# Kernel tuning notes

Hardware: AMD Instinct MI355X
Metric: run time of the kernel (lower is better)

The kernel has to match this reference:

```python
import jax, jax.numpy as jnp
import numpy as np

D_MODEL = 1024
NUM_HEADS = 16


def setup_inputs() -> dict:
    key = jax.random.key(0)
    ks = jax.random.split(key, 9)
    B, S, D = 4, 1024, D_MODEL
    scale = 1.0 / np.sqrt(D)
    inp = {
        "query": jax.random.normal(ks[0], (B, S, D), dtype=jnp.float32),
        "key": jax.random.normal(ks[1], (B, S, D), dtype=jnp.float32),
        "value": jax.random.normal(ks[2], (B, S, D), dtype=jnp.float32),
        # causal mask: 1 = attend, 0 = blocked (masked_fill where mask==0)
        "mask": jnp.tril(jnp.ones((S, S), dtype=jnp.int32))[None, None, :, :],
        "Wq": jax.random.normal(ks[3], (D, D), dtype=jnp.float32) * scale,
        "Wk": jax.random.normal(ks[4], (D, D), dtype=jnp.float32) * scale,
        "Wv": jax.random.normal(ks[5], (D, D), dtype=jnp.float32) * scale,
        "Wo": jax.random.normal(ks[6], (D, D), dtype=jnp.float32) * scale,
        "bo": jnp.zeros((D,), dtype=jnp.float32),
    }
    return inp


def reference(query, key, value, mask, Wq, Wk, Wv, Wo, bo):
    B, S, D = query.shape
    H = NUM_HEADS
    dk = D // H
    # torch Linear: y = x @ W.T  (bias=False for q/k/v)
    def proj(x, W):
        return (x @ W.T).reshape(B, S, H, dk).transpose(0, 2, 1, 3)  # [B,H,S,dk]

    Q = proj(query, Wq)
    K = proj(key, Wk)
    V = proj(value, Wv)

    scores = jnp.einsum("bhqd,bhkd->bhqk", Q, K) / jnp.sqrt(
        jnp.asarray(dk, dtype=jnp.float32)
    )
    scores = jnp.where(mask == 0, jnp.asarray(-1e9, scores.dtype), scores)
    attn = jax.nn.softmax(scores, axis=-1)
    out = jnp.einsum("bhqk,bhkd->bhqd", attn, V)  # [B,H,S,dk]
    out = out.transpose(0, 2, 1, 3).reshape(B, S, D)
    return out @ Wo.T + bo
```

## Files before the change

### kernel.cpp

```cpp
#include <hip/hip_runtime.h>

typedef __bf16 bf16x8 __attribute__((ext_vector_type(8)));
typedef short  s16x8  __attribute__((ext_vector_type(8)));
typedef float  f32x4  __attribute__((ext_vector_type(4)));
typedef float  f32x16 __attribute__((ext_vector_type(16)));
typedef unsigned int   u32x4 __attribute__((ext_vector_type(4)));
typedef unsigned short u16x4 __attribute__((ext_vector_type(4)));

#define NH   16
#define HD   64
#define SEQ  1024
#define DM   1024
#define NB   4
#define MTOT 4096

#define SCALE_L2E 0.1803368801111204f

__device__ __forceinline__ unsigned short f2bf(float f) {
    unsigned u = __builtin_bit_cast(unsigned, f);
    u += 0x7FFFu + ((u >> 16) & 1u);
    return (unsigned short)(u >> 16);
}

__device__ __forceinline__ s16x8 cvt8(f32x4 a, f32x4 b) {
    s16x8 r;
    r[0] = (short)f2bf(a[0]); r[1] = (short)f2bf(a[1]);
    r[2] = (short)f2bf(a[2]); r[3] = (short)f2bf(a[3]);
    r[4] = (short)f2bf(b[0]); r[5] = (short)f2bf(b[1]);
    r[6] = (short)f2bf(b[2]); r[7] = (short)f2bf(b[3]);
    return r;
}

__device__ __forceinline__ unsigned short bfbits(float x) {
    __bf16 h = (__bf16)x;
    return __builtin_bit_cast(unsigned short, h);
}
__device__ __forceinline__ float bf2f(unsigned short b) {
    unsigned u = (unsigned)b << 16;
    return __builtin_bit_cast(float, u);
}
__device__ __forceinline__ unsigned pk2(float a, float b) {
    return (unsigned)bfbits(a) | ((unsigned)bfbits(b) << 16);
}

__device__ __forceinline__ void gl16(const void* g, void* l) {
    __builtin_amdgcn_global_load_lds(
        (const __attribute__((address_space(1))) unsigned int*)g,
        (__attribute__((address_space(3))) unsigned int*)l, 16, 0, 0);
}

__device__ __forceinline__ bf16x8 ldfrag(const char* base, int row, int cb) {
    return __builtin_bit_cast(bf16x8,
        *(const s16x8*)(base + row * 128 + (cb ^ ((row & 7) << 4))));
}

__global__ __launch_bounds__(256)
void cvt_kernel(const float* __restrict__ q, const float* __restrict__ k,
                const float* __restrict__ v, const float* __restrict__ wq,
                const float* __restrict__ wk, const float* __restrict__ wv,
                unsigned short* __restrict__ dq, unsigned short* __restrict__ dk,
                unsigned short* __restrict__ dv, unsigned short* __restrict__ dwq,
                unsigned short* __restrict__ dwk, unsigned short* __restrict__ dwv)
{
    const int id = blockIdx.x;
    const float* s; unsigned short* d; int off; float scl = 1.0f;
    if (id < 6144) {
        const int t = id >> 11; off = id & 2047;
        s = (t == 0) ? q : (t == 1) ? k : v;
        d = (t == 0) ? dq : (t == 1) ? dk : dv;
    } else {
        const int w = (id - 6144) >> 9; off = (id - 6144) & 511;
        s = (w == 0) ? wq : (w == 1) ? wk : wv;
        d = (w == 0) ? dwq : (w == 1) ? dwk : dwv;
        if (w == 0) scl = SCALE_L2E;
    }
    const int idx = off * 2048 + threadIdx.x * 8;
    const f32x4* sp = (const f32x4*)(s + idx);
    *(s16x8*)(d + idx) = cvt8(sp[0] * scl, sp[1] * scl);
}

__device__ __forceinline__ void stage_half(const unsigned short* __restrict__ src,
                                           int grow0, int k0, char* ldsdst, int tid)
{
    const int wv  = tid >> 6;
    const int row = tid >> 3;
    const int scx = ((tid & 7) * 16) ^ ((row & 7) << 4);
    gl16((const char*)(src + (size_t)(grow0 + row) * DM + k0) + scx,
         ldsdst + wv * 1024);
    gl16((const char*)(src + (size_t)(grow0 + 64 + row) * DM + k0) + scx,
         ldsdst + 8192 + wv * 1024);
}

__device__ __forceinline__ void stage128x64(const unsigned short* __restrict__ src,
                                            int row0, int k0, char* lds, int tid)
{
    const int wv  = tid >> 6;
    const int row = tid >> 3;
    const int scx = ((tid & 7) * 16) ^ ((row & 7) << 4);
    #pragma unroll
    for (int i = 0; i < 4; ++i) {
        const char* g = (const char*)(src + (size_t)(row0 + i * 32 + row) * DM + k0) + scx;
        gl16(g, lds + i * 4096 + wv * 1024);
    }
}

__device__ __forceinline__ void loadB256(const float* __restrict__ src, int row0,
                                         int k0, int tid, f32x4 v[8])
{
    const int ce = (tid & 7) * 8;
    #pragma unroll
    for (int i = 0; i < 4; ++i) {
        const int row = (tid >> 3) + i * 32;
        const f32x4* p = (const f32x4*)(src + (size_t)(row0 + row) * DM + k0 + ce);
        v[2 * i] = p[0]; v[2 * i + 1] = p[1];
    }
}
__device__ __forceinline__ void writeB256(char* dst, int tid, const f32x4 v[8])
{
    const int cB = (tid & 7) * 16;
    #pragma unroll
    for (int i = 0; i < 4; ++i) {
        const int row = (tid >> 3) + i * 32;
        *(s16x8*)(dst + row * 128 + (cB ^ ((row & 7) << 4))) = cvt8(v[2 * i], v[2 * i + 1]);
    }
}

__global__ __launch_bounds__(512, 2)
void proj_kernel(const unsigned short* __restrict__ Xq,
                 const unsigned short* __restrict__ Xk,
                 const unsigned short* __restrict__ Xv,
                 const unsigned short* __restrict__ Wq,
                 const unsigned short* __restrict__ Wk,
                 const unsigned short* __restrict__ Wv,
                 unsigned short* __restrict__ Qo, unsigned short* __restrict__ Ko,
                 unsigned short* __restrict__ VTo)
{
    __shared__ char smem[147456];

    const int bid = blockIdx.x;
    const int swz = (bid & 7) * 24 + (bid >> 3);
    const int which = swz >> 6;
    const int rem   = swz & 63;
    const int m0 = (rem >> 2) * 256, n0 = (rem & 3) * 256;

    const unsigned short* X = (which == 0) ? Xq : (which == 1) ? Xk : Xv;
    const unsigned short* W = (which == 0) ? Wq : (which == 1) ? Wk : Wv;

    const int tid = threadIdx.x, lane = tid & 63, wv = tid >> 6;
    const int wrB = (wv >> 2) * 128;
    const int wcB = (wv & 3) * 64;
    const int fr = lane & 15, hi = lane >> 4, r4 = hi * 4;

    f32x4 acc[8][4];
    #pragma unroll
    for (int i = 0; i < 8; ++i)
        #pragma unroll
        for (int j = 0; j < 4; ++j) acc[i][j] = (f32x4){0.f, 0.f, 0.f, 0.f};

    stage_half(X, m0,       0, smem +     0, tid);
    stage_half(X, m0 + 128, 0, smem + 16384, tid);
    stage_half(W, n0,       0, smem + 32768, tid);
    stage_half(W, n0 + 128, 0, smem + 49152, tid);

    for (int t = 0; t < 16; ++t) {
        const char* Abuf = smem + (t & 1) * 65536;
        const char* Bbuf = Abuf + 32768;
        char* nb = smem + ((t & 1) ^ 1) * 65536;
        const int kn = (t + 1) * 64;

        bf16x8 af[2][4], bf01[2][2], bf23[2][2];

        if (t < 15) {
            stage_half(X, m0, kn, nb, tid);
            asm volatile("s_waitcnt vmcnt(2)" ::: "memory");
        } else {
            asm volatile("s_waitcnt vmcnt(0)" ::: "memory");
        }
        __builtin_amdgcn_s_barrier();
        __builtin_amdgcn_sched_barrier(0);
        #pragma unroll
        for (int ks = 0; ks < 2; ++ks) {
            const int cb = ks * 64 + hi * 16;
            #pragma unroll
            for (int mt = 0; mt < 4; ++mt) af[ks][mt] = ldfrag(Abuf, wrB + mt * 16 + fr, cb);
            #pragma unroll
            for (int nt = 0; nt < 2; ++nt) bf01[ks][nt] = ldfrag(Bbuf, wcB + nt * 16 + fr, cb);
        }
        __builtin_amdgcn_s_setprio(1);
        #pragma unroll
        for (int ks = 0; ks < 2; ++ks)
            #pragma unroll
            for (int mt = 0; mt < 4; ++mt)
                #pragma unroll
                for (int nt = 0; nt < 2; ++nt)
                    acc[mt][nt] = __builtin_amdgcn_mfma_f32_16x16x32_bf16(
                        af[ks][mt], bf01[ks][nt], acc[mt][nt], 0, 0, 0);
        __builtin_amdgcn_s_setprio(0);

        __builtin_amdgcn_s_barrier();
        __builtin_amdgcn_sched_barrier(0);
        #pragma unroll
        for (int ks = 0; ks < 2; ++ks) {
            const int cb = ks * 64 + hi * 16;
            #pragma unroll
            for (int nt = 0; nt < 2; ++nt) bf23[ks][nt] = ldfrag(Bbuf, wcB + 32 + nt * 16 + fr, cb);
        }
        if (t < 15) stage_half(X, m0 + 128, kn, nb + 16384, tid);
        __builtin_amdgcn_s_setprio(1);
        #pragma unroll
        for (int ks = 0; ks < 2; ++ks)
            #pragma unroll
            for (int mt = 0; mt < 4; ++mt)
                #pragma unroll
                for (int nt = 0; nt < 2; ++nt)
                    acc[mt][nt + 2] = __builtin_amdgcn_mfma_f32_16x16x32_bf16(
                        af[ks][mt], bf23[ks][nt], acc[mt][nt + 2], 0, 0, 0);
        __builtin_amdgcn_s_setprio(0);

        __builtin_amdgcn_s_barrier();
        __builtin_amdgcn_sched_barrier(0);
        #pragma unroll
        for (int ks = 0; ks < 2; ++ks) {
            const int cb = ks * 64 + hi * 16;
            #pragma unroll
            for (int mt = 0; mt < 4; ++mt) af[ks][mt] = ldfrag(Abuf, wrB + 64 + mt * 16 + fr, cb);
        }
        if (t < 15) stage_half(W, n0, kn, nb + 32768, tid);
        __builtin_amdgcn_s_setprio(1);
        #pragma unroll
        for (int ks = 0; ks < 2; ++ks)
            #pragma unroll
            for (int mt = 0; mt < 4; ++mt)
                #pragma unroll
                for (int nt = 0; nt < 2; ++nt)
                    acc[mt + 4][nt] = __builtin_amdgcn_mfma_f32_16x16x32_bf16(
                        af[ks][mt], bf01[ks][nt], acc[mt + 4][nt], 0, 0, 0);
        __builtin_amdgcn_s_setprio(0);

        __builtin_amdgcn_s_barrier();
        __builtin_amdgcn_sched_barrier(0);
        if (t < 15) stage_half(W, n0 + 128, kn, nb + 49152, tid);
        __builtin_amdgcn_s_setprio(1);
        #pragma unroll
        for (int ks = 0; ks < 2; ++ks)
            #pragma unroll
            for (int mt = 0; mt < 4; ++mt)
                #pragma unroll
                for (int nt = 0; nt < 2; ++nt)
                    acc[mt + 4][nt + 2] = __builtin_amdgcn_mfma_f32_16x16x32_bf16(
                        af[ks][mt], bf23[ks][nt], acc[mt + 4][nt + 2], 0, 0, 0);
        __builtin_amdgcn_s_setprio(0);
    }

    __syncthreads();

    unsigned short* sE = (unsigned short*)(smem + wv * 18432);
    #pragma unroll
    for (int mt = 0; mt < 8; ++mt)
        #pragma unroll
        for (int nt = 0; nt < 4; ++nt)
            #pragma unroll
            for (int r = 0; r < 4; ++r) {
                const int row = mt * 16 + r4 + r;
                const int col = nt * 16 + fr;
                sE[row * 72 + (col ^ (((row >> 3) & 7) << 3))] = f2bf(acc[mt][nt][r]);
            }
    asm volatile("s_waitcnt lgkmcnt(0)" ::: "memory");

    const int hB    = (n0 + wcB) >> 6;
    const int sbase = m0 + wrB;
    const int bb    = sbase >> 10;
    const int srow0 = sbase & 1023;

    if (which < 2) {
        unsigned short* QK = ((which == 0) ? Qo : Ko)
            + (((size_t)(bb * NH + hB)) * SEQ + srow0) * HD;
        #pragma unroll
        for (int it = 0; it < 16; ++it) {
            const int idx = it * 64 + lane;
            const int row = idx >> 3, c = idx & 7;
            s16x8 v = *(const s16x8*)&sE[row * 72 + ((c ^ ((row >> 3) & 7)) * 8)];
            *(s16x8*)(QK + (size_t)row * HD + c * 8) = v;
        }
    } else {
        const int t0 = srow0 >> 6;
        unsigned short* VD = VTo + (size_t)(bb * NH + hB) * (SEQ * HD)
                                 + (size_t)t0 * 4096;
        #pragma unroll
        for (int it = 0; it < 16; ++it) {
            const int tt = it >> 3, r = it & 7;
            const int sb = tt * 64 + (r >> 1) * 16 + (lane >> 5) * 8;
            const int d  = (lane & 31) + (r & 1) * 32;
            s16x8 v;
            #pragma unroll
            for (int j = 0; j < 8; ++j) {
                const int row = sb + j;
                v[j] = (short)sE[row * 72 + (d ^ (((row >> 3) & 7) << 3))];
            }
            *(s16x8*)(VD + (size_t)(tt * 8 + r) * 512 + lane * 8) = v;
        }
    }
}

__global__ __launch_bounds__(256)
void outproj_kernel(const unsigned short* __restrict__ A,
                    const float* __restrict__ Wo,
                    const float* __restrict__ bo,
                    float* __restrict__ Cout)
{
    const int bid = blockIdx.x;
    const int swz = (bid & 7) * 32 + (bid >> 3);
    const int m0 = (swz >> 3) * 128, n0 = (swz & 7) * 128;

    __shared__ char sA[2][16384];
    __shared__ char sB[2][16384];

    const int tid = threadIdx.x, lane = tid & 63, wv = tid >> 6;
    const int wr = (wv >> 1) * 64, wc = (wv & 1) * 64;
    const int fr = lane & 15, hi = lane >> 4, r4 = hi * 4;

    f32x4 acc[4][4];
    #pragma unroll
    for (int i = 0; i < 4; ++i)
        #pragma unroll
        for (int j = 0; j < 4; ++j) acc[i][j] = (f32x4){0.f, 0.f, 0.f, 0.f};

    f32x4 bv[8];
    loadB256(Wo, n0, 0, tid, bv);
    stage128x64(A, m0, 0, sA[0], tid);
    writeB256(sB[0], tid, bv);
    __syncthreads();

    for (int kt = 0; kt < 16; ++kt) {
        const int cur = kt & 1;
        if (kt < 15) {
            loadB256(Wo, n0, (kt + 1) * 64, tid, bv);
            stage128x64(A, m0, (kt + 1) * 64, sA[cur ^ 1], tid);
            asm volatile("s_waitcnt vmcnt(12)" ::: "memory");
        } else {
            asm volatile("s_waitcnt vmcnt(0)" ::: "memory");
        }
        __builtin_amdgcn_s_barrier();
        __builtin_amdgcn_sched_barrier(0);
        #pragma unroll
        for (int ks = 0; ks < 2; ++ks) {
            const int cb = ks * 64 + hi * 16;
            bf16x8 af[4], bfm[4];
            #pragma unroll
            for (int mt = 0; mt < 4; ++mt)
                af[mt] = ldfrag(sA[cur], wr + mt * 16 + fr, cb);
            #pragma unroll
            for (int nt = 0; nt < 4; ++nt)
                bfm[nt] = ldfrag(sB[cur], wc + nt * 16 + fr, cb);
            #pragma unroll
            for (int mt = 0; mt < 4; ++mt)
                #pragma unroll
                for (int nt = 0; nt < 4; ++nt)
                    acc[mt][nt] = __builtin_amdgcn_mfma_f32_16x16x32_bf16(
                        af[mt], bfm[nt], acc[mt][nt], 0, 0, 0);
        }
        if (kt < 15) writeB256(sB[cur ^ 1], tid, bv);
        asm volatile("s_waitcnt lgkmcnt(0)" ::: "memory");
        __builtin_amdgcn_sched_barrier(0);
        __builtin_amdgcn_s_barrier();
    }

    #pragma unroll
    for (int mt = 0; mt < 4; ++mt)
        #pragma unroll
        for (int nt = 0; nt < 4; ++nt)
            #pragma unroll
            for (int r = 0; r < 4; ++r) {
                int gm = m0 + wr + mt * 16 + r4 + r;
                int gn = n0 + wc + nt * 16 + fr;
                Cout[(size_t)gm * DM + gn] = acc[mt][nt][r] + bo[gn];
            }
}

__device__ __forceinline__ void stageK64(const char* Kc, int t, char* myK, int lane) {
    const int krow8 = lane >> 3;
    const int kcol  = ((lane & 7) * 16) ^ (krow8 << 4);
    const char* kb = Kc + (size_t)t * 8192;
    #pragma unroll
    for (int i = 0; i < 8; ++i)
        gl16(kb + (i * 8 + krow8) * 128 + kcol, myK + i * 1024);
}

__global__ __launch_bounds__(256)
void attn_kernel(const unsigned short* __restrict__ Q,
                 const unsigned short* __restrict__ K,
                 const unsigned short* __restrict__ VT,
                 unsigned short* __restrict__ O)
{
    __shared__ char smem[4][8192];

    const int bid = blockIdx.x;
    const int xcd = bid & 7, idx = bid >> 3;
    const int bh  = xcd * 8 + (idx & 7);
    const int rb  = 15 - (idx >> 3);
    const int tid = threadIdx.x, lane = tid & 63, wv = tid >> 6;
    const int g = wv >> 1, p = wv & 1;
    const int q0w = rb * 64 + g * 32;
    const int ql = lane & 31, hi = lane >> 5;
    const int qg = q0w + ql;
    const int ndiag = q0w >> 6;

    char* myK = smem[wv];

    const unsigned short* Qp = Q + (size_t)bh * SEQ * HD;
    const char* Kc  = (const char*)(K  + (size_t)bh * SEQ * HD);
    const char* Vfc = (const char*)(VT + (size_t)bh * SEQ * HD);

    bf16x8 qf[4];
    #pragma unroll
    for (int s = 0; s < 4; ++s)
        qf[s] = __builtin_bit_cast(bf16x8,
            *(const s16x8*)(Qp + (size_t)qg * HD + s * 16 + hi * 8));

    f32x16 o0, o1;
    #pragma unroll
    for (int i = 0; i < 16; ++i) { o0[i] = 0.f; o1[i] = 0.f; }
    float mrow = -3.0e38f, lrow = 0.f;

    if (p <= ndiag) stageK64(Kc, p, myK, lane);

    for (int t = p; t <= ndiag; t += 2) {
        asm volatile("s_waitcnt vmcnt(0)" ::: "memory");
        __builtin_amdgcn_sched_barrier(0);

        f32x16 s0, s1;
        #pragma unroll
        for (int i = 0; i < 16; ++i) { s0[i] = 0.f; s1[i] = 0.f; }
        #pragma unroll
        for (int s = 0; s < 4; ++s) {
            const int cb = s * 32 + hi * 16;
            bf16x8 k0 = ldfrag(myK, ql, cb);
            bf16x8 k1 = ldfrag(myK, 32 + ql, cb);
            s0 = __builtin_amdgcn_mfma_f32_32x32x16_bf16(k0, qf[s], s0, 0, 0, 0);
            s1 = __builtin_amdgcn_mfma_f32_32x32x16_bf16(k1, qf[s], s1, 0, 0, 0);
        }
        asm volatile("s_waitcnt lgkmcnt(0)" ::: "memory");
        __builtin_amdgcn_sched_barrier(0);

        const char* vb = Vfc + (size_t)t * 8192;
        s16x8 vr[8];
        #pragma unroll
        for (int r = 0; r < 8; ++r)
            vr[r] = *(const s16x8*)(vb + r * 1024 + lane * 16);
        if (t + 2 <= ndiag) stageK64(Kc, t + 2, myK, lane);

        if (t == ndiag) {
            #pragma unroll
            for (int r = 0; r < 16; ++r) {
                const int kl = t * 64 + (r & 3) + 8 * (r >> 2) + 4 * hi;
                s0[r] = (kl      <= qg) ? s0[r] : -3.0e38f;
                s1[r] = (kl + 32 <= qg) ? s1[r] : -3.0e38f;
            }
        }

        float mt = s0[0];
        #pragma unroll
        for (int r = 1; r < 16; ++r) mt = fmaxf(mt, s0[r]);
        #pragma unroll
        for (int r = 0; r < 16; ++r) mt = fmaxf(mt, s1[r]);
        mt = fmaxf(mt, __shfl_xor(mt, 32, 64));

        if (!__all(mt - mrow <= 8.0f)) {
            const float mnew = fmaxf(mrow, mt);
            const float pc = __builtin_amdgcn_exp2f(mrow - mnew);
            mrow = mnew;
            lrow *= pc;
            #pragma unroll
            for (int i = 0; i < 16; ++i) { o0[i] *= pc; o1[i] *= pc; }
        }

        float ts = 0.f;
        #pragma unroll
        for (int r = 0; r < 16; ++r) { s0[r] = __builtin_amdgcn_exp2f(s0[r] - mrow); ts += s0[r]; }
        #pragma unroll
        for (int r = 0; r < 16; ++r) { s1[r] = __builtin_amdgcn_exp2f(s1[r] - mrow); ts += s1[r]; }
        ts += __shfl_xor(ts, 32, 64);
        lrow += ts;

        #pragma unroll
        for (int s = 0; s < 4; ++s) {
            const f32x16 ps = (s < 2) ? s0 : s1;
            const int bse = (s & 1) * 8;
            unsigned w0 = pk2(ps[bse + 0], ps[bse + 1]);
            unsigned w1 = pk2(ps[bse + 2], ps[bse + 3]);
            unsigned w2 = pk2(ps[bse + 4], ps[bse + 5]);
            unsigned w3 = pk2(ps[bse + 6], ps[bse + 7]);
            unsigned x0 = (unsigned)__shfl_xor((int)(hi ? w0 : w2), 32, 64);
            unsigned x1 = (unsigned)__shfl_xor((int)(hi ? w1 : w3), 32, 64);
            u32x4 fw;
            fw[0] = hi ? x0 : w0;
            fw[1] = hi ? x1 : w1;
            fw[2] = hi ? w2 : x0;
            fw[3] = hi ? w3 : x1;
            const bf16x8 pfrag = __builtin_bit_cast(bf16x8, fw);
            o0 = __builtin_amdgcn_mfma_f32_32x32x16_bf16(
                __builtin_bit_cast(bf16x8, vr[2 * s]), pfrag, o0, 0, 0, 0);
            o1 = __builtin_amdgcn_mfma_f32_32x32x16_bf16(
                __builtin_bit_cast(bf16x8, vr[2 * s + 1]), pfrag, o1, 0, 0, 0);
        }
    }

    if (p == 1) {
        unsigned* rec = (unsigned*)smem[wv] + lane * 21;
        #pragma unroll
        for (int i = 0; i < 8; ++i) rec[i]     = pk2(o0[2 * i], o0[2 * i + 1]);
        #pragma unroll
        for (int i = 0; i < 8; ++i) rec[8 + i] = pk2(o1[2 * i], o1[2 * i + 1]);
        rec[16] = __builtin_bit_cast(unsigned, mrow);
        rec[17] = __builtin_bit_cast(unsigned, lrow);
        asm volatile("s_waitcnt lgkmcnt(0)" ::: "memory");
    }
    __syncthreads();
    if (p == 0) {
        const unsigned* rec = (const unsigned*)smem[wv + 1] + lane * 21;
        const float m1 = __builtin_bit_cast(float, rec[16]);
        const float l1 = __builtin_bit_cast(float, rec[17]);
        const float ms = fmaxf(mrow, m1);
        const float c0 = __builtin_amdgcn_exp2f(mrow - ms);
        const float c1 = __builtin_amdgcn_exp2f(m1 - ms);
        const float inv = 1.0f / (lrow * c0 + l1 * c1);
        const float a0 = c0 * inv, a1 = c1 * inv;

        unsigned short* sE = (unsigned short*)smem[wv];
        #pragma unroll
        for (int dt = 0; dt < 2; ++dt) {
            const f32x16 ov = dt ? o1 : o0;
            #pragma unroll
            for (int j = 0; j < 4; ++j) {
                u16x4 w;
                #pragma unroll
                for (int i = 0; i < 4; ++i) {
                    const int ii = 4 * j + i;
                    const unsigned uw = rec[dt * 8 + (ii >> 1)];
                    const float pv = bf2f((unsigned short)((ii & 1) ? (uw >> 16) : (uw & 0xffff)));
                    w[i] = bfbits(ov[ii] * a0 + pv * a1);
                }
                *(u16x4*)&sE[ql * 72 + dt * 32 + 8 * j + 4 * hi] = w;
            }
        }
        asm volatile("s_waitcnt lgkmcnt(0)" ::: "memory");
        const int bb = bh >> 4, h = bh & 15;
        #pragma unroll
        for (int it = 0; it < 4; ++it) {
            const int ix = it * 64 + lane;
            const int qq = ix >> 3, c = ix & 7;
            s16x8 v = *(const s16x8*)&sE[qq * 72 + c * 8];
            *(s16x8*)(O + ((size_t)(bb * SEQ + q0w + qq) * DM + h * 64) + c * 8) = v;
        }
    }
}

extern "C" void kernel_launch(void* const* d_in, const int* in_sizes, int n_in,
                              void* d_out, int out_size, void* d_ws, size_t ws_size,
                              hipStream_t stream)
{
    const float* query = (const float*)d_in[0];
    const float* key   = (const float*)d_in[1];
    const float* value = (const float*)d_in[2];
    const float* Wq = (const float*)d_in[4];
    const float* Wk = (const float*)d_in[5];
    const float* Wv = (const float*)d_in[6];
    const float* Wo = (const float*)d_in[7];
    const float* bo = (const float*)d_in[8];
    float* out = (float*)d_out;

    const size_t XE = (size_t)MTOT * DM;
    const size_t WE = (size_t)DM * DM;
    unsigned short* ws16 = (unsigned short*)d_ws;
    unsigned short* Xq16 = ws16;
    unsigned short* Xk16 = Xq16 + XE;
    unsigned short* Xv16 = Xk16 + XE;
    unsigned short* Wq16 = Xv16 + XE;
    unsigned short* Wk16 = Wq16 + WE;
    unsigned short* Wv16 = Wk16 + WE;
    unsigned short* Qw   = Wv16 + WE;
    unsigned short* Kw   = Qw + XE;
    unsigned short* VTw  = Kw + XE;
    unsigned short* AO   = VTw + XE;

    cvt_kernel<<<dim3(7680), dim3(256), 0, stream>>>(
        query, key, value, Wq, Wk, Wv,
        Xq16, Xk16, Xv16, Wq16, Wk16, Wv16);

    proj_kernel<<<dim3(192), dim3(512), 0, stream>>>(
        Xq16, Xk16, Xv16, Wq16, Wk16, Wv16, Qw, Kw, VTw);

    attn_kernel<<<dim3(1024), dim3(256), 0, stream>>>(Qw, Kw, VTw, AO);

    outproj_kernel<<<dim3(256), dim3(256), 0, stream>>>(AO, Wo, bo, out);
}
```

Measured before the change: 98.18 us.

## Pre-convert Wo to bf16 and stage it via async LDS loads; reorder attention V loads

Wo is now converted to bf16 in the existing conversion kernel, which gets more blocks. The output projection can then stage both operands with direct global-to-LDS loads instead of loading fp32 into registers and converting into LDS every iteration. In the attention kernel, the V fragment loads move ahead of the QK MFMAs and s_setprio raises wave priority around the MFMA blocks, so the loads overlap with compute. In exchange, the conversion kernel does extra work and Wo takes more workspace.

Measured after the change: 96.21 us. 2.0% less time.

```diff
diff --git a/kernel.cpp b/kernel.cpp
--- a/kernel.cpp
+++ b/kernel.cpp
@@ -58,9 +58,11 @@
 void cvt_kernel(const float* __restrict__ q, const float* __restrict__ k,
                 const float* __restrict__ v, const float* __restrict__ wq,
                 const float* __restrict__ wk, const float* __restrict__ wv,
+                const float* __restrict__ wo,
                 unsigned short* __restrict__ dq, unsigned short* __restrict__ dk,
                 unsigned short* __restrict__ dv, unsigned short* __restrict__ dwq,
-                unsigned short* __restrict__ dwk, unsigned short* __restrict__ dwv)
+                unsigned short* __restrict__ dwk, unsigned short* __restrict__ dwv,
+                unsigned short* __restrict__ dwo)
 {
     const int id = blockIdx.x;
     const float* s; unsigned short* d; int off; float scl = 1.0f;
@@ -70,8 +72,8 @@
         d = (t == 0) ? dq : (t == 1) ? dk : dv;
     } else {
         const int w = (id - 6144) >> 9; off = (id - 6144) & 511;
-        s = (w == 0) ? wq : (w == 1) ? wk : wv;
-        d = (w == 0) ? dwq : (w == 1) ? dwk : dwv;
+        s = (w == 0) ? wq : (w == 1) ? wk : (w == 2) ? wv : wo;
+        d = (w == 0) ? dwq : (w == 1) ? dwk : (w == 2) ? dwv : dwo;
         if (w == 0) scl = SCALE_L2E;
     }
     const int idx = off * 2048 + threadIdx.x * 8;
@@ -101,27 +103,6 @@
     for (int i = 0; i < 4; ++i) {
         const char* g = (const char*)(src + (size_t)(row0 + i * 32 + row) * DM + k0) + scx;
         gl16(g, lds + i * 4096 + wv * 1024);
-    }
-}
-
-__device__ __forceinline__ void loadB256(const float* __restrict__ src, int row0,
-                                         int k0, int tid, f32x4 v[8])
-{
-    const int ce = (tid & 7) * 8;
-    #pragma unroll
-    for (int i = 0; i < 4; ++i) {
-        const int row = (tid >> 3) + i * 32;
-        const f32x4* p = (const f32x4*)(src + (size_t)(row0 + row) * DM + k0 + ce);
-        v[2 * i] = p[0]; v[2 * i + 1] = p[1];
-    }
-}
-__device__ __forceinline__ void writeB256(char* dst, int tid, const f32x4 v[8])
-{
-    const int cB = (tid & 7) * 16;
-    #pragma unroll
-    for (int i = 0; i < 4; ++i) {
-        const int row = (tid >> 3) + i * 32;
-        *(s16x8*)(dst + row * 128 + (cB ^ ((row & 7) << 4))) = cvt8(v[2 * i], v[2 * i + 1]);
     }
 }
 
@@ -304,7 +285,7 @@
 
 __global__ __launch_bounds__(256)
 void outproj_kernel(const unsigned short* __restrict__ A,
-                    const float* __restrict__ Wo,
+                    const unsigned short* __restrict__ Wo,
                     const float* __restrict__ bo,
                     float* __restrict__ Cout)
 {
@@ -325,18 +306,15 @@
         #pragma unroll
         for (int j = 0; j < 4; ++j) acc[i][j] = (f32x4){0.f, 0.f, 0.f, 0.f};
 
-    f32x4 bv[8];
-    loadB256(Wo, n0, 0, tid, bv);
-    stage128x64(A, m0, 0, sA[0], tid);
-    writeB256(sB[0], tid, bv);
-    __syncthreads();
+    stage128x64(A,  m0, 0, sA[0], tid);
+    stage128x64(Wo, n0, 0, sB[0], tid);
 
     for (int kt = 0; kt < 16; ++kt) {
         const int cur = kt & 1;
         if (kt < 15) {
-            loadB256(Wo, n0, (kt + 1) * 64, tid, bv);
-            stage128x64(A, m0, (kt + 1) * 64, sA[cur ^ 1], tid);
-            asm volatile("s_waitcnt vmcnt(12)" ::: "memory");
+            stage128x64(A,  m0, (kt + 1) * 64, sA[cur ^ 1], tid);
+            stage128x64(Wo, n0, (kt + 1) * 64, sB[cur ^ 1], tid);
+            asm volatile("s_waitcnt vmcnt(8)" ::: "memory");
         } else {
             asm volatile("s_waitcnt vmcnt(0)" ::: "memory");
         }
@@ -359,7 +337,6 @@
                     acc[mt][nt] = __builtin_amdgcn_mfma_f32_16x16x32_bf16(
                         af[mt], bfm[nt], acc[mt][nt], 0, 0, 0);
         }
-        if (kt < 15) writeB256(sB[cur ^ 1], tid, bv);
         asm volatile("s_waitcnt lgkmcnt(0)" ::: "memory");
         __builtin_amdgcn_sched_barrier(0);
         __builtin_amdgcn_s_barrier();
@@ -428,9 +405,17 @@
         asm volatile("s_waitcnt vmcnt(0)" ::: "memory");
         __builtin_amdgcn_sched_barrier(0);
 
+        const char* vb = Vfc + (size_t)t * 8192;
+        s16x8 vr[8];
+        #pragma unroll
+        for (int r = 0; r < 8; ++r)
+            vr[r] = *(const s16x8*)(vb + r * 1024 + lane * 16);
+        __builtin_amdgcn_sched_barrier(0);
+
         f32x16 s0, s1;
         #pragma unroll
         for (int i = 0; i < 16; ++i) { s0[i] = 0.f; s1[i] = 0.f; }
+        __builtin_amdgcn_s_setprio(1);
         #pragma unroll
         for (int s = 0; s < 4; ++s) {
             const int cb = s * 32 + hi * 16;
@@ -439,14 +424,10 @@
             s0 = __builtin_amdgcn_mfma_f32_32x32x16_bf16(k0, qf[s], s0, 0, 0, 0);
             s1 = __builtin_amdgcn_mfma_f32_32x32x16_bf16(k1, qf[s], s1, 0, 0, 0);
         }
+        __builtin_amdgcn_s_setprio(0);
         asm volatile("s_waitcnt lgkmcnt(0)" ::: "memory");
         __builtin_amdgcn_sched_barrier(0);
 
-        const char* vb = Vfc + (size_t)t * 8192;
-        s16x8 vr[8];
-        #pragma unroll
-        for (int r = 0; r < 8; ++r)
-            vr[r] = *(const s16x8*)(vb + r * 1024 + lane * 16);
         if (t + 2 <= ndiag) stageK64(Kc, t + 2, myK, lane);
 
         if (t == ndiag) {
@@ -498,10 +479,12 @@
             fw[2] = hi ? w2 : x0;
             fw[3] = hi ? w3 : x1;
             const bf16x8 pfrag = __builtin_bit_cast(bf16x8, fw);
+            __builtin_amdgcn_s_setprio(1);
             o0 = __builtin_amdgcn_mfma_f32_32x32x16_bf16(
                 __builtin_bit_cast(bf16x8, vr[2 * s]), pfrag, o0, 0, 0, 0);
             o1 = __builtin_amdgcn_mfma_f32_32x32x16_bf16(
                 __builtin_bit_cast(bf16x8, vr[2 * s + 1]), pfrag, o1, 0, 0, 0);
+            __builtin_amdgcn_s_setprio(0);
         }
     }
 
@@ -578,19 +561,20 @@
     unsigned short* Wq16 = Xv16 + XE;
     unsigned short* Wk16 = Wq16 + WE;
     unsigned short* Wv16 = Wk16 + WE;
-    unsigned short* Qw   = Wv16 + WE;
+    unsigned short* Wo16 = Wv16 + WE;
+    unsigned short* Qw   = Wo16 + WE;
     unsigned short* Kw   = Qw + XE;
     unsigned short* VTw  = Kw + XE;
     unsigned short* AO   = VTw + XE;
 
-    cvt_kernel<<<dim3(7680), dim3(256), 0, stream>>>(
-        query, key, value, Wq, Wk, Wv,
-        Xq16, Xk16, Xv16, Wq16, Wk16, Wv16);
+    cvt_kernel<<<dim3(8192), dim3(256), 0, stream>>>(
+        query, key, value, Wq, Wk, Wv, Wo,
+        Xq16, Xk16, Xv16, Wq16, Wk16, Wv16, Wo16);
 
     proj_kernel<<<dim3(192), dim3(512), 0, stream>>>(
         Xq16, Xk16, Xv16, Wq16, Wk16, Wv16, Qw, Kw, VTw);
 
     attn_kernel<<<dim3(1024), dim3(256), 0, stream>>>(Qw, Kw, VTw, AO);
 
-    outproj_kernel<<<dim3(256), dim3(256), 0, stream>>>(AO, Wo, bo, out);
-}
+    outproj_kernel<<<dim3(256), dim3(256), 0, stream>>>(AO, Wo16, bo, out);
+}
```
